# Kernel tuning notes

Measured on AMD Instinct MI355X. Metric: run time of the kernel, lower is better.

## Reference

```python
import jax, jax.numpy as jnp
import numpy as np

TOKENS = 8192
IN_FEATURES = 4096
OUT_FEATURES = 4096
ALPHA = 2e-05
BETA = 8.0


def setup_inputs() -> dict:
    key = jax.random.key(0)
    kx, kw = jax.random.split(key)
    # int8 activations and weights, values in [-127, 127]
    x = jax.random.randint(kx, (TOKENS, IN_FEATURES), -127, 128, dtype=jnp.int32).astype(jnp.int8)
    weight = jax.random.randint(kw, (OUT_FEATURES, IN_FEATURES), -127, 128, dtype=jnp.int32).astype(jnp.int8)
    bias = jnp.zeros((OUT_FEATURES,), dtype=jnp.float32)
    a = jnp.float32(ALPHA)  # dequant scale: input_scale * weight_scale
    b = jnp.float32(BETA)   # requant scale: 1 / out_scale
    return {"x": x, "weight": weight, "bias": bias, "a": a, "b": b}


def reference(x, weight, bias, a, b):
    acc = jnp.matmul(x.astype(jnp.int32), weight.T.astype(jnp.int32))
    # fp32 epilogue: dequant scale + bias, exact GeLU, requant by beta
    y = a * acc.astype(jnp.float32) + bias[None, :]
    y = jax.nn.gelu(y, approximate=False)
    # quantize output to int8 (round to nearest even, saturate)
    q = jnp.clip(jnp.rint(y * b), -128.0, 127.0).astype(jnp.int8)
    return q
```

## Files before the change

### kernel.cpp

```cpp
#include <hip/hip_runtime.h>
#include <cstdint>
#include <cstddef>

#define TOKENS 8192
#define INF    4096
#define OUTF   4096

typedef int v4i __attribute__((ext_vector_type(4)));

__global__ __launch_bounds__(256) void pack_i8_kernel(
    const int* __restrict__ xi, const int* __restrict__ wi,
    uint8_t* __restrict__ x8, uint8_t* __restrict__ w8) {
  const int NX = (TOKENS * INF) / 4;
  const int NT = 2048 * 256;
  int tid = blockIdx.x * 256 + threadIdx.x;
#pragma unroll 1
  for (int g = 0; g < 6; ++g) {
    int c[4];
    int4 v[4];
#pragma unroll
    for (int j = 0; j < 4; ++j) {
      c[j] = (g * 4 + j) * NT + tid;
      const int4* src = (c[j] < NX) ? ((const int4*)xi + c[j])
                                    : ((const int4*)wi + (c[j] - NX));
      v[j] = *src;
    }
#pragma unroll
    for (int j = 0; j < 4; ++j) {
      unsigned* dst = (c[j] < NX) ? ((unsigned*)x8 + c[j])
                                  : ((unsigned*)w8 + (c[j] - NX));
      *dst = (v[j].x & 255) | ((v[j].y & 255) << 8) | ((v[j].z & 255) << 16) |
             (((unsigned)v[j].w) << 24);
    }
  }
}

__device__ __forceinline__ float gelu_exact(float y) {
  float x = y * 0.70710678118654752f;
  float s = fabsf(x);
  float t = __builtin_amdgcn_rcpf(fmaf(s, 0.3275911f, 1.0f));
  float p = t * fmaf(t, fmaf(t, fmaf(t, fmaf(t, 1.061405429f, -1.453152027f),
                                     1.421413741f), -0.284496736f),
                     0.254829592f);
  float e = __expf(-s * s);
  float er = fmaf(-p, e, 1.0f);
  er = copysignf(er, x);
  return 0.5f * y * (1.0f + er);
}

__device__ __forceinline__ void barrier_fenced() {
  asm volatile("" ::: "memory");
  __builtin_amdgcn_s_barrier();
  asm volatile("" ::: "memory");
}

__global__ __launch_bounds__(512, 2) void gemm_i8_gelu_q_kernel(
    const uint8_t* __restrict__ x8, const uint8_t* __restrict__ w8,
    const float* __restrict__ bias, const float* __restrict__ pa,
    const float* __restrict__ pb, int* __restrict__ out) {
  __shared__ char sm[131072];

  const int tid = threadIdx.x;
  const int l   = tid & 63;
  const int wv  = tid >> 6;
  const int wr  = wv >> 2;
  const int wc  = wv & 3;
  const int lr  = l & 15;
  const int lg  = l >> 4;

  int id = blockIdx.x;
  int wg = (id & 7) * 64 + (id >> 3);
  const int m0 = (wg >> 4) * 256;
  const int n0 = (wg & 15) * 256;

  const float av = pa[0];
  const float bv = pb[0];

  const int srow4 = l >> 2;
  const int schu  = ((l & 3) ^ (srow4 & 3)) << 4;
  const uint8_t* bA = x8 + (size_t)(m0 + wv * 16 + srow4) * INF + schu;
  const uint8_t* bB = w8 + (size_t)(n0 + wv * 16 + srow4) * INF + schu;
  const int dA = wv * 1024;

  int aoff[8], boff[4];
#pragma unroll
  for (int m = 0; m < 8; ++m)
    aoff[m] = (wr * 128 + m * 16 + lr) * 64 + ((lg ^ (lr & 3)) << 4);
#pragma unroll
  for (int n = 0; n < 4; ++n)
    boff[n] = 65536 + (wc * 64 + n * 16 + lr) * 64 + ((lg ^ (lr & 3)) << 4);

  v4i acc[8][4];
#pragma unroll
  for (int m = 0; m < 8; ++m)
#pragma unroll
    for (int n = 0; n < 4; ++n) acc[m][n] = (v4i){0, 0, 0, 0};

#define GLL(gsrc, ldst)                                                       \
  __builtin_amdgcn_global_load_lds(                                           \
      (const __attribute__((address_space(1))) unsigned*)(gsrc),              \
      (__attribute__((address_space(3))) unsigned*)(ldst), 16, 0, 0);

#define GLA(H, J) GLL(bA + (size_t)(H) * 64 + (size_t)(J) * 128 * INF,        \
                      sm + (((H) & 3) << 14) + (J) * 8192 + dA)
#define GLB(H, J) GLL(bB + (size_t)(H) * 64 + (size_t)(J) * 128 * INF,        \
                      sm + 65536 + (((H) & 3) << 14) + (J) * 8192 + dA)

#define MM(m, n) acc[m][n] = __builtin_amdgcn_mfma_i32_16x16x64_i8(           \
                     Af[m], Bf[n], acc[m][n], 0, 0, 0)

#define PRE_MFMA                                                              \
  barrier_fenced();                                                           \
  asm volatile("s_waitcnt lgkmcnt(0)" ::: "memory");                          \
  __builtin_amdgcn_s_setprio(1);
#define POST_MFMA                                                             \
  __builtin_amdgcn_s_setprio(0);                                              \
  barrier_fenced();

#define HALF(H, S, DOSTAGE, NW)                                               \
  {                                                                           \
    const char* sb_ = sm + ((S) << 14);                                       \
    v4i Af[8], Bf[4];                                                         \
                                        \
    Af[0] = *(const v4i*)(sb_ + aoff[0]);                                     \
    Af[1] = *(const v4i*)(sb_ + aoff[1]);                                     \
    Af[2] = *(const v4i*)(sb_ + aoff[2]);                                     \
    Af[3] = *(const v4i*)(sb_ + aoff[3]);                                     \
    Bf[0] = *(const v4i*)(sb_ + boff[0]);                                     \
    Bf[1] = *(const v4i*)(sb_ + boff[1]);                                     \
    if (DOSTAGE) { GLA((H) + 3, 0); }                                         \
    PRE_MFMA                                                                  \
    MM(0, 0); MM(0, 1); MM(1, 0); MM(1, 1);                                   \
    MM(2, 0); MM(2, 1); MM(3, 0); MM(3, 1);                                   \
    POST_MFMA                                                                 \
                                             \
    Af[4] = *(const v4i*)(sb_ + aoff[4]);                                     \
    Af[5] = *(const v4i*)(sb_ + aoff[5]);                                     \
    Af[6] = *(const v4i*)(sb_ + aoff[6]);                                     \
    Af[7] = *(const v4i*)(sb_ + aoff[7]);                                     \
    if (DOSTAGE) { GLA((H) + 3, 1); }                                         \
    PRE_MFMA                                                                  \
    MM(4, 0); MM(4, 1); MM(5, 0); MM(5, 1);                                   \
    MM(6, 0); MM(6, 1); MM(7, 0); MM(7, 1);                                   \
    POST_MFMA                                                                 \
                                             \
    Bf[2] = *(const v4i*)(sb_ + boff[2]);                                     \
    Bf[3] = *(const v4i*)(sb_ + boff[3]);                                     \
    if (DOSTAGE) { GLB((H) + 3, 0); }                                         \
    PRE_MFMA                                                                  \
    MM(0, 2); MM(0, 3); MM(1, 2); MM(1, 3);                                   \
    MM(2, 2); MM(2, 3); MM(3, 2); MM(3, 3);                                   \
    POST_MFMA                                                                 \
           \
    if (DOSTAGE) { GLB((H) + 3, 1); }                                         \
    barrier_fenced();                                                         \
    __builtin_amdgcn_s_setprio(1);                                            \
    MM(4, 2); MM(4, 3); MM(5, 2); MM(5, 3);                                   \
    MM(6, 2); MM(6, 3); MM(7, 2); MM(7, 3);                                   \
    __builtin_amdgcn_s_setprio(0);                                            \
    if ((NW) == 8) { asm volatile("s_waitcnt vmcnt(8)" ::: "memory"); }       \
    else if ((NW) == 4) { asm volatile("s_waitcnt vmcnt(4)" ::: "memory"); }  \
    else if ((NW) == 0) { asm volatile("s_waitcnt vmcnt(0)" ::: "memory"); }  \
    if ((NW) >= 0) { barrier_fenced(); }                                      \
  }

#pragma unroll
  for (int hh = 0; hh < 3; ++hh) {
    GLA(hh, 0); GLA(hh, 1); GLB(hh, 0); GLB(hh, 1);
  }
  asm volatile("s_waitcnt vmcnt(8)" ::: "memory");
  barrier_fenced();

#pragma unroll 1
  for (int hb = 0; hb < 60; hb += 4) {
    HALF(hb + 0, 0, 1, 8)
    HALF(hb + 1, 1, 1, 8)
    HALF(hb + 2, 2, 1, 8)
    HALF(hb + 3, 3, 1, 8)
  }
  HALF(60, 0, 1, 8)
  HALF(61, 1, 0, 4)
  HALF(62, 2, 0, 0)
  HALF(63, 3, 0, -1)

  float bvals[4];
#pragma unroll
  for (int n = 0; n < 4; ++n) bvals[n] = bias[n0 + wc * 64 + n * 16 + lr];

#pragma unroll
  for (int m = 0; m < 8; ++m) {
    int rowb = m0 + wr * 128 + m * 16 + lg * 4;
#pragma unroll
    for (int q = 0; q < 4; ++q) {
      size_t rb = (size_t)(rowb + q) * OUTF;
#pragma unroll
      for (int n = 0; n < 4; ++n) {
        float f = fmaf(av, (float)acc[m][n][q], bvals[n]);
        float g = gelu_exact(f);
        float r = __builtin_rintf(g * bv);
        r = fminf(fmaxf(r, -128.0f), 127.0f);
        out[rb + (size_t)(n0 + wc * 64 + n * 16 + lr)] = (int)r;
      }
    }
  }
#undef GLL
#undef GLA
#undef GLB
#undef MM
#undef PRE_MFMA
#undef POST_MFMA
#undef HALF
}

extern "C" void kernel_launch(void* const* d_in, const int* in_sizes, int n_in,
                              void* d_out, int out_size, void* d_ws,
                              size_t ws_size, hipStream_t stream) {
  const int*   xi   = (const int*)d_in[0];
  const int*   wi   = (const int*)d_in[1];
  const float* bias = (const float*)d_in[2];
  const float* pa   = (const float*)d_in[3];
  const float* pb   = (const float*)d_in[4];
  int*         out  = (int*)d_out;

  uint8_t* x8 = (uint8_t*)d_ws;
  uint8_t* w8 = x8 + (size_t)TOKENS * INF;

  pack_i8_kernel<<<2048, 256, 0, stream>>>(xi, wi, x8, w8);

  dim3 grid((TOKENS / 256) * (OUTF / 256));
  gemm_i8_gelu_q_kernel<<<grid, 512, 0, stream>>>(x8, w8, bias, pa, pb, out);
}
```

Baseline: 411.9 us.

## Switch GEMM mainloop to double-buffered 128-byte K tiles with 8-way swizzle

Replaces the 4-stage ring of 64-byte-wide K slices (3 in flight) with a 2-stage double buffer of 128-byte K tiles, changes the LDS swizzle to an 8-chunk XOR pattern, and cuts the loop to 32 iterations of two MFMA K-steps each. The aim is fewer barriers and waits per unit of K and wider global-to-LDS rows. The cost is shallower prefetch: only one tile is in flight, and each iteration ends with a full vmcnt(0) wait, so global latency may be less hidden.

```diff
diff --git a/kernel.cpp b/kernel.cpp
--- a/kernel.cpp
+++ b/kernel.cpp
@@ -76,19 +76,19 @@
   const float av = pa[0];
   const float bv = pb[0];
 
-  const int srow4 = l >> 2;
-  const int schu  = ((l & 3) ^ (srow4 & 3)) << 4;
-  const uint8_t* bA = x8 + (size_t)(m0 + wv * 16 + srow4) * INF + schu;
-  const uint8_t* bB = w8 + (size_t)(n0 + wv * 16 + srow4) * INF + schu;
-  const int dA = wv * 1024;
-
-  int aoff[8], boff[4];
-#pragma unroll
-  for (int m = 0; m < 8; ++m)
-    aoff[m] = (wr * 128 + m * 16 + lr) * 64 + ((lg ^ (lr & 3)) << 4);
-#pragma unroll
-  for (int n = 0; n < 4; ++n)
-    boff[n] = 65536 + (wc * 64 + n * 16 + lr) * 64 + ((lg ^ (lr & 3)) << 4);
+  const int grow = (wv << 5) + (l >> 3);
+  const int gch  = ((l & 7) ^ ((l >> 3) & 7)) << 4;
+  const uint8_t* gA = x8 + (size_t)(m0 + grow) * INF + gch;
+  const uint8_t* gB = w8 + (size_t)(n0 + grow) * INF + gch;
+  const int dwv = wv * 4096;
+
+  int aoff[8], boff[4], sb0, sb1;
+#pragma unroll
+  for (int m = 0; m < 8; ++m) aoff[m] = (wr * 128 + m * 16 + lr) * 128;
+#pragma unroll
+  for (int n = 0; n < 4; ++n) boff[n] = 32768 + (wc * 64 + n * 16 + lr) * 128;
+  sb0 = ((0 + lg) ^ (l & 7)) << 4;
+  sb1 = ((4 + lg) ^ (l & 7)) << 4;
 
   v4i acc[8][4];
 #pragma unroll
@@ -101,87 +101,108 @@
       (const __attribute__((address_space(1))) unsigned*)(gsrc),              \
       (__attribute__((address_space(3))) unsigned*)(ldst), 16, 0, 0);
 
-#define GLA(H, J) GLL(bA + (size_t)(H) * 64 + (size_t)(J) * 128 * INF,        \
-                      sm + (((H) & 3) << 14) + (J) * 8192 + dA)
-#define GLB(H, J) GLL(bB + (size_t)(H) * 64 + (size_t)(J) * 128 * INF,        \
-                      sm + 65536 + (((H) & 3) << 14) + (J) * 8192 + dA)
-
-#define MM(m, n) acc[m][n] = __builtin_amdgcn_mfma_i32_16x16x64_i8(           \
-                     Af[m], Bf[n], acc[m][n], 0, 0, 0)
-
-#define PRE_MFMA                                                              \
+#define GLA(T, J) GLL(gA + (size_t)(J) * 8 * INF + (size_t)(T) * 128,         \
+                      sm + (((T) & 1) << 16) + dwv + (J) * 1024)
+#define GLB(T, J) GLL(gB + (size_t)(J) * 8 * INF + (size_t)(T) * 128,         \
+                      sm + (((T) & 1) << 16) + 32768 + dwv + (J) * 1024)
+
+#define LD(off) (*(const v4i*)(sbr + (off)))
+#define MM(ACC, AF, BF)                                                       \
+  ACC = __builtin_amdgcn_mfma_i32_16x16x64_i8(AF, BF, ACC, 0, 0, 0)
+
+#define PH_BAR                                                                \
   barrier_fenced();                                                           \
   asm volatile("s_waitcnt lgkmcnt(0)" ::: "memory");                          \
   __builtin_amdgcn_s_setprio(1);
-#define POST_MFMA                                                             \
-  __builtin_amdgcn_s_setprio(0);                                              \
+#define PH_END __builtin_amdgcn_s_setprio(0);
+
+#define ITER(DS)                                                              \
+  {                                                                           \
+    const char* sbr = sm + ((kt & 1) << 16);                                  \
+    const int T = kt + 1;                                                     \
+    v4i A0[4], A4[4], B0[2], B2[2];                                           \
+                                           \
+    A0[0] = LD(aoff[0] + sb0); A0[1] = LD(aoff[1] + sb0);                     \
+    A0[2] = LD(aoff[2] + sb0); A0[3] = LD(aoff[3] + sb0);                     \
+    B0[0] = LD(boff[0] + sb0); B0[1] = LD(boff[1] + sb0);                     \
+    if (DS) { GLA(T, 0); GLA(T, 1); }                                         \
+    PH_BAR                                               \
+    MM(acc[0][0], A0[0], B0[0]); MM(acc[0][1], A0[0], B0[1]);                 \
+    MM(acc[1][0], A0[1], B0[0]); MM(acc[1][1], A0[1], B0[1]);                 \
+    MM(acc[2][0], A0[2], B0[0]); MM(acc[2][1], A0[2], B0[1]);                 \
+    MM(acc[3][0], A0[3], B0[0]); MM(acc[3][1], A0[3], B0[1]);                 \
+    PH_END                                                                    \
+    A4[0] = LD(aoff[4] + sb0); A4[1] = LD(aoff[5] + sb0);                     \
+    A4[2] = LD(aoff[6] + sb0); A4[3] = LD(aoff[7] + sb0);                     \
+    if (DS) { GLA(T, 2); GLA(T, 3); }                                         \
+    PH_BAR                                               \
+    MM(acc[4][0], A4[0], B0[0]); MM(acc[4][1], A4[0], B0[1]);                 \
+    MM(acc[5][0], A4[1], B0[0]); MM(acc[5][1], A4[1], B0[1]);                 \
+    MM(acc[6][0], A4[2], B0[0]); MM(acc[6][1], A4[2], B0[1]);                 \
+    MM(acc[7][0], A4[3], B0[0]); MM(acc[7][1], A4[3], B0[1]);                 \
+    PH_END                                                                    \
+    B2[0] = LD(boff[2] + sb0); B2[1] = LD(boff[3] + sb0);                     \
+    if (DS) { GLB(T, 0); GLB(T, 1); }                                         \
+    PH_BAR                                               \
+    MM(acc[0][2], A0[0], B2[0]); MM(acc[0][3], A0[0], B2[1]);                 \
+    MM(acc[1][2], A0[1], B2[0]); MM(acc[1][3], A0[1], B2[1]);                 \
+    MM(acc[2][2], A0[2], B2[0]); MM(acc[2][3], A0[2], B2[1]);                 \
+    MM(acc[3][2], A0[3], B2[0]); MM(acc[3][3], A0[3], B2[1]);                 \
+    PH_END                                                                    \
+    if (DS) { GLB(T, 2); GLB(T, 3); }                                         \
+    PH_BAR                                               \
+    MM(acc[4][2], A4[0], B2[0]); MM(acc[4][3], A4[0], B2[1]);                 \
+    MM(acc[5][2], A4[1], B2[0]); MM(acc[5][3], A4[1], B2[1]);                 \
+    MM(acc[6][2], A4[2], B2[0]); MM(acc[6][3], A4[2], B2[1]);                 \
+    MM(acc[7][2], A4[3], B2[0]); MM(acc[7][3], A4[3], B2[1]);                 \
+    PH_END                                                                    \
+                              \
+    A0[0] = LD(aoff[0] + sb1); A0[1] = LD(aoff[1] + sb1);                     \
+    A0[2] = LD(aoff[2] + sb1); A0[3] = LD(aoff[3] + sb1);                     \
+    B0[0] = LD(boff[0] + sb1); B0[1] = LD(boff[1] + sb1);                     \
+    PH_BAR                                                            \
+    MM(acc[0][0], A0[0], B0[0]); MM(acc[0][1], A0[0], B0[1]);                 \
+    MM(acc[1][0], A0[1], B0[0]); MM(acc[1][1], A0[1], B0[1]);                 \
+    MM(acc[2][0], A0[2], B0[0]); MM(acc[2][1], A0[2], B0[1]);                 \
+    MM(acc[3][0], A0[3], B0[0]); MM(acc[3][1], A0[3], B0[1]);                 \
+    PH_END                                                                    \
+    A4[0] = LD(aoff[4] + sb1); A4[1] = LD(aoff[5] + sb1);                     \
+    A4[2] = LD(aoff[6] + sb1); A4[3] = LD(aoff[7] + sb1);                     \
+    PH_BAR                                                            \
+    MM(acc[4][0], A4[0], B0[0]); MM(acc[4][1], A4[0], B0[1]);                 \
+    MM(acc[5][0], A4[1], B0[0]); MM(acc[5][1], A4[1], B0[1]);                 \
+    MM(acc[6][0], A4[2], B0[0]); MM(acc[6][1], A4[2], B0[1]);                 \
+    MM(acc[7][0], A4[3], B0[0]); MM(acc[7][1], A4[3], B0[1]);                 \
+    PH_END                                                                    \
+    B2[0] = LD(boff[2] + sb1); B2[1] = LD(boff[3] + sb1);                     \
+    PH_BAR                                                            \
+    MM(acc[0][2], A0[0], B2[0]); MM(acc[0][3], A0[0], B2[1]);                 \
+    MM(acc[1][2], A0[1], B2[0]); MM(acc[1][3], A0[1], B2[1]);                 \
+    MM(acc[2][2], A0[2], B2[0]); MM(acc[2][3], A0[2], B2[1]);                 \
+    MM(acc[3][2], A0[3], B2[0]); MM(acc[3][3], A0[3], B2[1]);                 \
+    PH_END                                                                    \
+    PH_BAR                                                            \
+    MM(acc[4][2], A4[0], B2[0]); MM(acc[4][3], A4[0], B2[1]);                 \
+    MM(acc[5][2], A4[1], B2[0]); MM(acc[5][3], A4[1], B2[1]);                 \
+    MM(acc[6][2], A4[2], B2[0]); MM(acc[6][3], A4[2], B2[1]);                 \
+    MM(acc[7][2], A4[3], B2[0]); MM(acc[7][3], A4[3], B2[1]);                 \
+    PH_END                                                                    \
+                  \
+    if (DS) { asm volatile("s_waitcnt vmcnt(0)" ::: "memory"); }              \
+    barrier_fenced();                                                         \
+  }
+
+  GLA(0, 0); GLA(0, 1); GLA(0, 2); GLA(0, 3);
+  GLB(0, 0); GLB(0, 1); GLB(0, 2); GLB(0, 3);
+  asm volatile("s_waitcnt vmcnt(0)" ::: "memory");
   barrier_fenced();
 
-#define HALF(H, S, DOSTAGE, NW)                                               \
-  {                                                                           \
-    const char* sb_ = sm + ((S) << 14);                                       \
-    v4i Af[8], Bf[4];                                                         \
-                                        \
-    Af[0] = *(const v4i*)(sb_ + aoff[0]);                                     \
-    Af[1] = *(const v4i*)(sb_ + aoff[1]);                                     \
-    Af[2] = *(const v4i*)(sb_ + aoff[2]);                                     \
-    Af[3] = *(const v4i*)(sb_ + aoff[3]);                                     \
-    Bf[0] = *(const v4i*)(sb_ + boff[0]);                                     \
-    Bf[1] = *(const v4i*)(sb_ + boff[1]);                                     \
-    if (DOSTAGE) { GLA((H) + 3, 0); }                                         \
-    PRE_MFMA                                                                  \
-    MM(0, 0); MM(0, 1); MM(1, 0); MM(1, 1);                                   \
-    MM(2, 0); MM(2, 1); MM(3, 0); MM(3, 1);                                   \
-    POST_MFMA                                                                 \
-                                             \
-    Af[4] = *(const v4i*)(sb_ + aoff[4]);                                     \
-    Af[5] = *(const v4i*)(sb_ + aoff[5]);                                     \
-    Af[6] = *(const v4i*)(sb_ + aoff[6]);                                     \
-    Af[7] = *(const v4i*)(sb_ + aoff[7]);                                     \
-    if (DOSTAGE) { GLA((H) + 3, 1); }                                         \
-    PRE_MFMA                                                                  \
-    MM(4, 0); MM(4, 1); MM(5, 0); MM(5, 1);                                   \
-    MM(6, 0); MM(6, 1); MM(7, 0); MM(7, 1);                                   \
-    POST_MFMA                                                                 \
-                                             \
-    Bf[2] = *(const v4i*)(sb_ + boff[2]);                                     \
-    Bf[3] = *(const v4i*)(sb_ + boff[3]);                                     \
-    if (DOSTAGE) { GLB((H) + 3, 0); }                                         \
-    PRE_MFMA                                                                  \
-    MM(0, 2); MM(0, 3); MM(1, 2); MM(1, 3);                                   \
-    MM(2, 2); MM(2, 3); MM(3, 2); MM(3, 3);                                   \
-    POST_MFMA                                                                 \
-           \
-    if (DOSTAGE) { GLB((H) + 3, 1); }                                         \
-    barrier_fenced();                                                         \
-    __builtin_amdgcn_s_setprio(1);                                            \
-    MM(4, 2); MM(4, 3); MM(5, 2); MM(5, 3);                                   \
-    MM(6, 2); MM(6, 3); MM(7, 2); MM(7, 3);                                   \
-    __builtin_amdgcn_s_setprio(0);                                            \
-    if ((NW) == 8) { asm volatile("s_waitcnt vmcnt(8)" ::: "memory"); }       \
-    else if ((NW) == 4) { asm volatile("s_waitcnt vmcnt(4)" ::: "memory"); }  \
-    else if ((NW) == 0) { asm volatile("s_waitcnt vmcnt(0)" ::: "memory"); }  \
-    if ((NW) >= 0) { barrier_fenced(); }                                      \
-  }
-
-#pragma unroll
-  for (int hh = 0; hh < 3; ++hh) {
-    GLA(hh, 0); GLA(hh, 1); GLB(hh, 0); GLB(hh, 1);
-  }
-  asm volatile("s_waitcnt vmcnt(8)" ::: "memory");
-  barrier_fenced();
-
 #pragma unroll 1
-  for (int hb = 0; hb < 60; hb += 4) {
-    HALF(hb + 0, 0, 1, 8)
-    HALF(hb + 1, 1, 1, 8)
-    HALF(hb + 2, 2, 1, 8)
-    HALF(hb + 3, 3, 1, 8)
-  }
-  HALF(60, 0, 1, 8)
-  HALF(61, 1, 0, 4)
-  HALF(62, 2, 0, 0)
-  HALF(63, 3, 0, -1)
+  for (int kt = 0; kt < 31; ++kt) ITER(1)
+  {
+    const int kt = 31;
+    ITER(0)
+  }
 
   float bvals[4];
 #pragma unroll
@@ -206,10 +227,11 @@
 #undef GLL
 #undef GLA
 #undef GLB
+#undef LD
 #undef MM
-#undef PRE_MFMA
-#undef POST_MFMA
-#undef HALF
+#undef PH_BAR
+#undef PH_END
+#undef ITER
 }
 
 extern "C" void kernel_launch(void* const* d_in, const int* in_sizes, int n_in,
```

Result: faster. 400.2 us (-2.8%).
